# Kernel tuning notes

Measured on AMD Instinct MI355X. Metric: run time of the kernel, lower is better.

## Reference

```python
import jax, jax.numpy as jnp
import numpy as np

D_MODEL = 1024
NUM_HEADS = 16


def setup_inputs() -> dict:
    key = jax.random.key(0)
    k1, k2, k3, k4, k5 = jax.random.split(key, 5)
    b, n, d = 4, 2048, D_MODEL
    s = 1.0 / np.sqrt(d)
    x = jax.random.normal(k1, (b, n, d), dtype=jnp.float32)
    v_w = jax.random.uniform(k2, (d, d), dtype=jnp.float32, minval=-s, maxval=s)  # Linear weight [out,in]
    v_b = jax.random.uniform(k3, (d,), dtype=jnp.float32, minval=-s, maxval=s)
    o_w = jax.random.uniform(k4, (d, d), dtype=jnp.float32, minval=-s, maxval=s)
    o_b = jax.random.uniform(k5, (d,), dtype=jnp.float32, minval=-s, maxval=s)
    return {"x": x, "v_w": v_w, "v_b": v_b, "o_w": o_w, "o_b": o_b}


def reference(x, v_w, v_b, o_w, o_b):
    b, n, d = x.shape
    h = NUM_HEADS
    dh = d // h
    # shared QKV projection: q = k = v
    v = jnp.einsum('bnd,ed->bne', x, v_w) + v_b            # [b,n,d]
    v = v.reshape(b, n, h, dh).transpose(0, 2, 1, 3)        # [b,h,n,dh]
    scale = 1.0 / jnp.sqrt(jnp.asarray(dh, dtype=x.dtype))
    scores = jnp.einsum('bhnd,bhmd->bhnm', v, v) * scale    # [b,h,n,n]
    attn = jax.nn.softmax(scores, axis=-1)
    out = jnp.einsum('bhnm,bhmd->bhnd', attn, v)            # [b,h,n,dh]
    out = out.transpose(0, 2, 1, 3).reshape(b, n, d)        # concat heads
    return jnp.einsum('bnd,ed->bne', out, o_w) + o_b
```

## Files before the change

### kernel.cpp

```cpp
#include <hip/hip_runtime.h>
#include <stdint.h>

typedef __attribute__((ext_vector_type(8))) short short8;
typedef __attribute__((ext_vector_type(4))) float f32x4;
typedef __attribute__((ext_vector_type(4))) unsigned int u32x4;
typedef __attribute__((ext_vector_type(2))) unsigned int u32x2;

#define MFMA16(a, b, c) __builtin_amdgcn_mfma_f32_16x16x32_bf16((a), (b), (c), 0, 0, 0)

#define GLD_LDS16(g, l)                                                                  \
    __builtin_amdgcn_global_load_lds((const __attribute__((address_space(1))) void*)(g), \
                                     (__attribute__((address_space(3))) void*)(l), 16, 0, 0)

#if defined(__has_builtin)
#if __has_builtin(__builtin_amdgcn_exp2f)
#define FAST_EXP2(x) __builtin_amdgcn_exp2f(x)
#endif
#endif
#ifndef FAST_EXP2
__device__ __forceinline__ float fast_exp2_asm(float x) {
    float r;
    asm volatile("v_exp_f32 %0, %1\ns_nop 1" : "=v"(r) : "v"(x));
    return r;
}
#define FAST_EXP2(x) fast_exp2_asm(x)
#endif

__device__ __forceinline__ float bf2f(unsigned short u) {
    unsigned int x = ((unsigned int)u) << 16;
    float f;
    __builtin_memcpy(&f, &x, 4);
    return f;
}
__device__ __forceinline__ unsigned short f2bf(float f) {
    unsigned int x;
    __builtin_memcpy(&x, &f, 4);
    unsigned int r = x + 0x7FFFu + ((x >> 16) & 1u);
    return (unsigned short)(r >> 16);
}
__device__ __forceinline__ unsigned int pack2bf(float a, float b) {
    unsigned int ua, ub;
    __builtin_memcpy(&ua, &a, 4);
    __builtin_memcpy(&ub, &b, 4);
    return __builtin_amdgcn_perm(ub + 0x8000u, ua + 0x8000u, 0x07060302u);
}
__device__ __forceinline__ u32x4 cvt8(const float* p) {
    f32x4 g0 = *(const f32x4*)p;
    f32x4 g1 = *(const f32x4*)(p + 4);
    u32x4 r;
    r.x = pack2bf(g0[0], g0[1]);
    r.y = pack2bf(g0[2], g0[3]);
    r.z = pack2bf(g1[0], g1[1]);
    r.w = pack2bf(g1[2], g1[3]);
    return r;
}

__global__ __launch_bounds__(256) void cvt_kernel(const float* __restrict__ in,
                                                  unsigned short* __restrict__ out, int n8) {
    int i = blockIdx.x * 256 + threadIdx.x;
    if (i < n8) *(u32x4*)(out + (size_t)i * 8) = cvt8(in + (size_t)i * 8);
}

template <int MODE>
__global__ __launch_bounds__(256) void gemm_dma_kernel(
    const unsigned short* __restrict__ A, const unsigned short* __restrict__ B,
    const float* __restrict__ bias, void* __restrict__ Cv, int M, int N, int K) {
    __shared__ __align__(16) unsigned short As[2][2][128 * 32];
    __shared__ __align__(16) unsigned short Bs[2][2][128 * 32];

    const int tid = threadIdx.x;
    const int wave = tid >> 6, lane = tid & 63;
    const int l15 = lane & 15, quad = lane >> 4;
    const int m0 = blockIdx.x * 128, n0 = blockIdx.y * 128;
    const int wm = (wave >> 1) * 64, wn = (wave & 1) * 64;

    const int row0 = tid >> 2, c0 = (tid & 3) * 8;
    const unsigned short* Ag0 = A + (size_t)(m0 + row0) * K + c0;
    const unsigned short* Ag1 = A + (size_t)(m0 + row0 + 64) * K + c0;
    const unsigned short* Bg0 = B + (size_t)(n0 + row0) * K + c0;
    const unsigned short* Bg1 = B + (size_t)(n0 + row0 + 64) * K + c0;
    const int wl = wave * 512;

#define STAGE(s, k0)                                     \
    do {                                                 \
        GLD_LDS16(Ag0 + (k0), &As[s][0][wl]);            \
        GLD_LDS16(Ag1 + (k0), &As[s][0][2048 + wl]);     \
        GLD_LDS16(Ag0 + (k0) + 32, &As[s][1][wl]);       \
        GLD_LDS16(Ag1 + (k0) + 32, &As[s][1][2048 + wl]); \
        GLD_LDS16(Bg0 + (k0), &Bs[s][0][wl]);            \
        GLD_LDS16(Bg1 + (k0), &Bs[s][0][2048 + wl]);     \
        GLD_LDS16(Bg0 + (k0) + 32, &Bs[s][1][wl]);       \
        GLD_LDS16(Bg1 + (k0) + 32, &Bs[s][1][2048 + wl]); \
    } while (0)

    f32x4 acc[4][4];
#pragma unroll
    for (int i = 0; i < 4; i++)
#pragma unroll
        for (int j = 0; j < 4; j++) {
            f32x4 z = {0.f, 0.f, 0.f, 0.f};
            acc[i][j] = z;
        }

    STAGE(0, 0);
    for (int k0 = 0; k0 < K; k0 += 64) {
        const int s = (k0 >> 6) & 1;
        __syncthreads();
        if (k0 + 64 < K) STAGE(s ^ 1, k0 + 64);

        short8 a0[4], a1[4], b0[4], b1[4];
#pragma unroll
        for (int mt = 0; mt < 4; mt++) {
            a0[mt] = *(const short8*)&As[s][0][(wm + mt * 16 + l15) * 32 + quad * 8];
            a1[mt] = *(const short8*)&As[s][1][(wm + mt * 16 + l15) * 32 + quad * 8];
        }
#pragma unroll
        for (int nt = 0; nt < 4; nt++) {
            b0[nt] = *(const short8*)&Bs[s][0][(wn + nt * 16 + l15) * 32 + quad * 8];
            b1[nt] = *(const short8*)&Bs[s][1][(wn + nt * 16 + l15) * 32 + quad * 8];
        }
#pragma unroll
        for (int mt = 0; mt < 4; mt++)
#pragma unroll
            for (int nt = 0; nt < 4; nt++) acc[mt][nt] = MFMA16(a0[mt], b0[nt], acc[mt][nt]);
#pragma unroll
        for (int mt = 0; mt < 4; mt++)
#pragma unroll
            for (int nt = 0; nt < 4; nt++) acc[mt][nt] = MFMA16(a1[mt], b1[nt], acc[mt][nt]);
    }
#undef STAGE

    float bv[4];
#pragma unroll
    for (int nt = 0; nt < 4; nt++) bv[nt] = bias[n0 + wn + nt * 16 + l15];

#pragma unroll
    for (int mt = 0; mt < 4; mt++)
#pragma unroll
        for (int nt = 0; nt < 4; nt++)
#pragma unroll
            for (int i = 0; i < 4; i++) {
                int m = m0 + wm + mt * 16 + quad * 4 + i;
                int n = n0 + wn + nt * 16 + l15;
                float val = acc[mt][nt][i] + bv[nt];
                if (MODE == 0) {
                    int bb = m >> 11, ns = m & 2047, h = n >> 6, c = n & 63;
                    ((unsigned short*)Cv)[(size_t)(bb * 16 + h) * 131072 + (size_t)ns * 64 + c] =
                        f2bf(val);
                } else {
                    ((float*)Cv)[(size_t)m * N + n] = val;
                }
            }
}

template <bool AF32, bool BF32, int MODE>
__global__ __launch_bounds__(256) void gemm_bias_kernel(
    const void* __restrict__ Av, const void* __restrict__ Bv,
    const float* __restrict__ bias, void* __restrict__ Cv, int M, int N, int K) {
    __shared__ __align__(16) unsigned short As[128][40];
    __shared__ __align__(16) unsigned short Bs[128][40];

    const int tid = threadIdx.x;
    const int wave = tid >> 6, lane = tid & 63;
    const int l15 = lane & 15, quad = lane >> 4;
    const int m0 = blockIdx.x * 128, n0 = blockIdx.y * 128;
    const int wm = (wave >> 1) * 64, wn = (wave & 1) * 64;

    f32x4 acc[4][4];
#pragma unroll
    for (int i = 0; i < 4; i++)
#pragma unroll
        for (int j = 0; j < 4; j++) {
            f32x4 z = {0.f, 0.f, 0.f, 0.f};
            acc[i][j] = z;
        }

    for (int k0 = 0; k0 < K; k0 += 32) {
        __syncthreads();
#pragma unroll
        for (int rep = 0; rep < 2; rep++) {
            int chunk = tid + rep * 256;
            int row = chunk >> 2, c8 = (chunk & 3) * 8;
            if (AF32) {
                const float* Af = (const float*)Av;
                *(u32x4*)&As[row][c8] = cvt8(&Af[(size_t)(m0 + row) * K + k0 + c8]);
            } else {
                const unsigned short* Ab = (const unsigned short*)Av;
                *(f32x4*)&As[row][c8] = *(const f32x4*)&Ab[(size_t)(m0 + row) * K + k0 + c8];
            }
            if (BF32) {
                const float* Bf = (const float*)Bv;
                *(u32x4*)&Bs[row][c8] = cvt8(&Bf[(size_t)(n0 + row) * K + k0 + c8]);
            } else {
                const unsigned short* Bb = (const unsigned short*)Bv;
                *(f32x4*)&Bs[row][c8] = *(const f32x4*)&Bb[(size_t)(n0 + row) * K + k0 + c8];
            }
        }
        __syncthreads();

        short8 a[4], b[4];
#pragma unroll
        for (int mt = 0; mt < 4; mt++) a[mt] = *(const short8*)&As[wm + mt * 16 + l15][quad * 8];
#pragma unroll
        for (int nt = 0; nt < 4; nt++) b[nt] = *(const short8*)&Bs[wn + nt * 16 + l15][quad * 8];
#pragma unroll
        for (int mt = 0; mt < 4; mt++)
#pragma unroll
            for (int nt = 0; nt < 4; nt++) acc[mt][nt] = MFMA16(a[mt], b[nt], acc[mt][nt]);
    }

    float bv[4];
#pragma unroll
    for (int nt = 0; nt < 4; nt++) bv[nt] = bias[n0 + wn + nt * 16 + l15];

#pragma unroll
    for (int mt = 0; mt < 4; mt++)
#pragma unroll
        for (int nt = 0; nt < 4; nt++)
#pragma unroll
            for (int i = 0; i < 4; i++) {
                int m = m0 + wm + mt * 16 + quad * 4 + i;
                int n = n0 + wn + nt * 16 + l15;
                float val = acc[mt][nt][i] + bv[nt];
                if (MODE == 0) {
                    int bb = m >> 11, ns = m & 2047, h = n >> 6, c = n & 63;
                    ((unsigned short*)Cv)[(size_t)(bb * 16 + h) * 131072 + (size_t)ns * 64 + c] =
                        f2bf(val);
                } else {
                    ((float*)Cv)[(size_t)m * N + n] = val;
                }
            }
}

__global__ __launch_bounds__(256) void transpose_kernel(const unsigned short* __restrict__ V,
                                                        unsigned short* __restrict__ Vt) {
    __shared__ __align__(16) unsigned short T[64][72];
    const int tid = threadIdx.x;
    const int n0 = blockIdx.x * 64;
    const size_t base = (size_t)blockIdx.y * 131072;
#pragma unroll
    for (int rep = 0; rep < 2; rep++) {
        int chunk = tid + rep * 256;
        int row = chunk >> 3, c8 = (chunk & 7) * 8;
        *(short8*)&T[row][c8] = *(const short8*)&V[base + (size_t)(n0 + row) * 64 + c8];
    }
    __syncthreads();
#pragma unroll
    for (int rep = 0; rep < 2; rep++) {
        int chunk = tid + rep * 256;
        int d = chunk >> 3, n8 = (chunk & 7) * 8;
        short8 o;
#pragma unroll
        for (int j = 0; j < 8; j++) o[j] = (short)T[n8 + j][d];
        *(short8*)&Vt[base + (size_t)d * 2048 + n0 + n8] = o;
    }
}

__global__ __launch_bounds__(256, 3) void attn_kernel(const unsigned short* __restrict__ V,
                                                      const unsigned short* __restrict__ Vt,
                                                      unsigned short* __restrict__ O) {
    __shared__ __align__(16) unsigned short QP[128 * 64];
    __shared__ __align__(16) unsigned short Ks[2][64 * 64];
    __shared__ __align__(16) unsigned short VTs[2][64 * 64];

    const int tid = threadIdx.x;
    const int wave = tid >> 6, lane = tid & 63;
    const int l15 = lane & 15, quad = lane >> 4;
    const int sx = l15 & 7;

    const int flat = blockIdx.y * 16 + blockIdx.x;
    const int bh = (flat & 7) * 8 + ((flat >> 3) & 7);
    const int q0 = (flat >> 6) * 128;

    const unsigned short* Vh = V + (size_t)bh * 131072;
    const unsigned short* VhT = Vt + (size_t)bh * 131072;
    const int wm = wave * 32;

    const int srow = wave * 16 + (lane >> 3);
    const int scol = ((lane & 7) ^ (lane >> 3)) * 8;
    const unsigned short* gK = Vh + (size_t)srow * 64 + scol;
    const unsigned short* gVT = VhT + (size_t)srow * 2048 + scol;

#define ASTAGE(s, kv)                                                       \
    do {                                                                    \
        GLD_LDS16(gK + (size_t)(kv) * 64, &Ks[s][wave * 1024]);             \
        GLD_LDS16(gK + (size_t)(kv) * 64 + 512, &Ks[s][wave * 1024 + 512]); \
        GLD_LDS16(gVT + (kv), &VTs[s][wave * 1024]);                        \
        GLD_LDS16(gVT + (kv) + 8 * 2048, &VTs[s][wave * 1024 + 512]);       \
    } while (0)

    ASTAGE(0, 0);

#pragma unroll
    for (int rep = 0; rep < 4; rep++) {
        int chunk = tid + rep * 256;
        int row = chunk >> 3, cs = chunk & 7;
        short8 g = *(const short8*)&Vh[(size_t)(q0 + row) * 64 + cs * 8];
        short8 o;
#pragma unroll
        for (int j = 0; j < 8; j++)
            o[j] = (short)f2bf(bf2f((unsigned short)g[j]) * 0.1803368801f);
        *(short8*)&QP[row * 64 + ((cs ^ (row & 7)) << 3)] = o;
    }
    __syncthreads();

    short8 bq[2][2];
#pragma unroll
    for (int mt = 0; mt < 2; mt++) {
        const int row = wm + mt * 16 + l15;
#pragma unroll
        for (int ks = 0; ks < 2; ks++)
            bq[mt][ks] = *(const short8*)&QP[row * 64 + ((((ks << 2) | quad) ^ sx) << 3)];
    }

    f32x4 oacc[2][4];
#pragma unroll
    for (int mt = 0; mt < 2; mt++)
#pragma unroll
        for (int ct = 0; ct < 4; ct++) {
            f32x4 z = {0.f, 0.f, 0.f, 0.f};
            oacc[mt][ct] = z;
        }
    float lsum[2] = {0.f, 0.f};

    for (int kv0 = 0; kv0 < 2048; kv0 += 64) {
        const int s = (kv0 >> 6) & 1;
        __syncthreads();
        if (kv0 + 64 < 2048) ASTAGE(s ^ 1, kv0 + 64);

        f32x4 st[4][2];
        __builtin_amdgcn_s_setprio(1);
#pragma unroll
        for (int nt = 0; nt < 4; nt++) {
            const int krow = (nt * 16 + l15) * 64;
            short8 ak0 = *(const short8*)&Ks[s][krow + ((quad ^ sx) << 3)];
            short8 ak1 = *(const short8*)&Ks[s][krow + (((4 | quad) ^ sx) << 3)];
#pragma unroll
            for (int mt = 0; mt < 2; mt++) {
                f32x4 z = {0.f, 0.f, 0.f, 0.f};
                z = MFMA16(ak0, bq[mt][0], z);
                z = MFMA16(ak1, bq[mt][1], z);
                st[nt][mt] = z;
            }
        }
        __builtin_amdgcn_s_setprio(0);

#pragma unroll
        for (int mt = 0; mt < 2; mt++) {
            const int prow = (wm + mt * 16 + l15) * 64;
#pragma unroll
            for (int nt = 0; nt < 4; nt++) {
                f32x4 p;
#pragma unroll
                for (int i = 0; i < 4; i++) p[i] = FAST_EXP2(st[nt][mt][i]);
                lsum[mt] += (p[0] + p[1]) + (p[2] + p[3]);
                u32x2 w;
                w.x = pack2bf(p[0], p[1]);
                w.y = pack2bf(p[2], p[3]);
                const int slot = (nt * 2 + (quad >> 1)) ^ sx;
                *(u32x2*)&QP[prow + slot * 8 + (quad & 1) * 4] = w;
            }
        }
        asm volatile("s_waitcnt lgkmcnt(0)" ::: "memory");

        __builtin_amdgcn_s_setprio(1);
#pragma unroll
        for (int kt = 0; kt < 2; kt++) {
            short8 ap[2];
#pragma unroll
            for (int mt = 0; mt < 2; mt++) {
                const int row = wm + mt * 16 + l15;
                ap[mt] = *(const short8*)&QP[row * 64 + ((((kt << 2) | quad) ^ sx) << 3)];
            }
#pragma unroll
            for (int ct = 0; ct < 4; ct++) {
                short8 bvf =
                    *(const short8*)&VTs[s][(ct * 16 + l15) * 64 + ((((kt << 2) | quad) ^ sx) << 3)];
#pragma unroll
                for (int mt = 0; mt < 2; mt++) oacc[mt][ct] = MFMA16(ap[mt], bvf, oacc[mt][ct]);
            }
        }
        __builtin_amdgcn_s_setprio(0);
    }
#undef ASTAGE

    float inv[2][4];
#pragma unroll
    for (int mt = 0; mt < 2; mt++) {
        float v = lsum[mt];
        v += __shfl_xor(v, 16, 64);
        v += __shfl_xor(v, 32, 64);
        float r = 1.0f / v;
#pragma unroll
        for (int i = 0; i < 4; i++) inv[mt][i] = __shfl(r, quad * 4 + i, 16);
    }

    const int bb = bh >> 4, h = bh & 15;
#pragma unroll
    for (int mt = 0; mt < 2; mt++)
#pragma unroll
        for (int i = 0; i < 4; i++) {
            int m = q0 + wm + mt * 16 + quad * 4 + i;
            size_t rowbase = ((size_t)(bb * 2048 + m)) * 1024 + h * 64;
#pragma unroll
            for (int ct = 0; ct < 4; ct++)
                O[rowbase + ct * 16 + l15] = f2bf(oacc[mt][ct][i] * inv[mt][i]);
        }
}

extern "C" void kernel_launch(void* const* d_in, const int* in_sizes, int n_in, void* d_out,
                              int out_size, void* d_ws, size_t ws_size, hipStream_t stream) {
    (void)in_sizes; (void)n_in; (void)out_size;
    const float* x = (const float*)d_in[0];
    const float* v_w = (const float*)d_in[1];
    const float* v_b = (const float*)d_in[2];
    const float* o_w = (const float*)d_in[3];
    const float* o_b = (const float*)d_in[4];
    float* out = (float*)d_out;

    unsigned short* Vbuf = (unsigned short*)d_out;
    unsigned short* Vtbuf = Vbuf + (size_t)8192 * 1024;
    unsigned short* Obuf = (unsigned short*)d_ws;

    const size_t need =
        ((size_t)8192 * 1024  + (size_t)8192 * 1024  + 2 * (size_t)1024 * 1024) * 2;
    if (ws_size >= need) {
        unsigned short* xbf = Obuf + (size_t)8192 * 1024;
        unsigned short* wv = xbf + (size_t)8192 * 1024;
        unsigned short* wo = wv + (size_t)1024 * 1024;
        cvt_kernel<<<4096, 256, 0, stream>>>(x, xbf, 1048576);
        cvt_kernel<<<512, 256, 0, stream>>>(v_w, wv, 131072);
        cvt_kernel<<<512, 256, 0, stream>>>(o_w, wo, 131072);
        gemm_dma_kernel<0><<<dim3(64, 8), 256, 0, stream>>>(xbf, wv, v_b, Vbuf, 8192, 1024, 1024);
        transpose_kernel<<<dim3(32, 64), 256, 0, stream>>>(Vbuf, Vtbuf);
        attn_kernel<<<dim3(16, 64), 256, 0, stream>>>(Vbuf, Vtbuf, Obuf);
        gemm_dma_kernel<1><<<dim3(64, 8), 256, 0, stream>>>(Obuf, wo, o_b, out, 8192, 1024, 1024);
    } else {
        gemm_bias_kernel<true, true, 0>
            <<<dim3(64, 8), 256, 0, stream>>>(x, v_w, v_b, Vbuf, 8192, 1024, 1024);
        transpose_kernel<<<dim3(32, 64), 256, 0, stream>>>(Vbuf, Vtbuf);
        attn_kernel<<<dim3(16, 64), 256, 0, stream>>>(Vbuf, Vtbuf, Obuf);
        gemm_bias_kernel<false, true, 1>
            <<<dim3(64, 8), 256, 0, stream>>>(Obuf, o_w, o_b, out, 8192, 1024, 1024);
    }
}
```

Baseline: 237.3 us.

## Single-buffer K tile with mid-iteration barrier to raise occupancy to four blocks

```diff
diff --git a/kernel.cpp b/kernel.cpp
--- a/kernel.cpp
+++ b/kernel.cpp
@@ -256,11 +256,11 @@
     }
 }
 
-__global__ __launch_bounds__(256, 3) void attn_kernel(const unsigned short* __restrict__ V,
+__global__ __launch_bounds__(256, 4) void attn_kernel(const unsigned short* __restrict__ V,
                                                       const unsigned short* __restrict__ Vt,
                                                       unsigned short* __restrict__ O) {
     __shared__ __align__(16) unsigned short QP[128 * 64];
-    __shared__ __align__(16) unsigned short Ks[2][64 * 64];
+    __shared__ __align__(16) unsigned short Ks[64 * 64];
     __shared__ __align__(16) unsigned short VTs[2][64 * 64];
 
     const int tid = threadIdx.x;
@@ -281,15 +281,19 @@
     const unsigned short* gK = Vh + (size_t)srow * 64 + scol;
     const unsigned short* gVT = VhT + (size_t)srow * 2048 + scol;
 
-#define ASTAGE(s, kv)                                                       \
-    do {                                                                    \
-        GLD_LDS16(gK + (size_t)(kv) * 64, &Ks[s][wave * 1024]);             \
-        GLD_LDS16(gK + (size_t)(kv) * 64 + 512, &Ks[s][wave * 1024 + 512]); \
-        GLD_LDS16(gVT + (kv), &VTs[s][wave * 1024]);                        \
-        GLD_LDS16(gVT + (kv) + 8 * 2048, &VTs[s][wave * 1024 + 512]);       \
+#define KSTAGE(kv)                                                       \
+    do {                                                                 \
+        GLD_LDS16(gK + (size_t)(kv) * 64, &Ks[wave * 1024]);             \
+        GLD_LDS16(gK + (size_t)(kv) * 64 + 512, &Ks[wave * 1024 + 512]); \
     } while (0)
-
-    ASTAGE(0, 0);
+#define VSTAGE(s, kv)                                                 \
+    do {                                                              \
+        GLD_LDS16(gVT + (kv), &VTs[s][wave * 1024]);                  \
+        GLD_LDS16(gVT + (kv) + 8 * 2048, &VTs[s][wave * 1024 + 512]); \
+    } while (0)
+
+    KSTAGE(0);
+    VSTAGE(0, 0);
 
 #pragma unroll
     for (int rep = 0; rep < 4; rep++) {
@@ -326,15 +330,14 @@
     for (int kv0 = 0; kv0 < 2048; kv0 += 64) {
         const int s = (kv0 >> 6) & 1;
         __syncthreads();
-        if (kv0 + 64 < 2048) ASTAGE(s ^ 1, kv0 + 64);
+        if (kv0 + 64 < 2048) VSTAGE(s ^ 1, kv0 + 64);
 
         f32x4 st[4][2];
-        __builtin_amdgcn_s_setprio(1);
 #pragma unroll
         for (int nt = 0; nt < 4; nt++) {
             const int krow = (nt * 16 + l15) * 64;
-            short8 ak0 = *(const short8*)&Ks[s][krow + ((quad ^ sx) << 3)];
-            short8 ak1 = *(const short8*)&Ks[s][krow + (((4 | quad) ^ sx) << 3)];
+            short8 ak0 = *(const short8*)&Ks[krow + ((quad ^ sx) << 3)];
+            short8 ak1 = *(const short8*)&Ks[krow + (((4 | quad) ^ sx) << 3)];
 #pragma unroll
             for (int mt = 0; mt < 2; mt++) {
                 f32x4 z = {0.f, 0.f, 0.f, 0.f};
@@ -343,7 +346,11 @@
                 st[nt][mt] = z;
             }
         }
-        __builtin_amdgcn_s_setprio(0);
+
+        __builtin_amdgcn_sched_barrier(0);
+        __builtin_amdgcn_s_barrier();
+        __builtin_amdgcn_sched_barrier(0);
+        if (kv0 + 64 < 2048) KSTAGE(kv0 + 64);
 
 #pragma unroll
         for (int mt = 0; mt < 2; mt++) {
@@ -363,7 +370,6 @@
         }
         asm volatile("s_waitcnt lgkmcnt(0)" ::: "memory");
 
-        __builtin_amdgcn_s_setprio(1);
 #pragma unroll
         for (int kt = 0; kt < 2; kt++) {
             short8 ap[2];
@@ -380,9 +386,9 @@
                 for (int mt = 0; mt < 2; mt++) oacc[mt][ct] = MFMA16(ap[mt], bvf, oacc[mt][ct]);
             }
         }
-        __builtin_amdgcn_s_setprio(0);
-    }
-#undef ASTAGE
+    }
+#undef KSTAGE
+#undef VSTAGE
 
     float inv[2][4];
 #pragma unroll
```

New measurement: 226.4 us. 1.05x faster.
